# Kernel tuning notes

Hardware: AMD Instinct MI355X
Metric: run time of the kernel (lower is better)

Reference implementation:

```python
import jax, jax.numpy as jnp
import numpy as np

N_NODES = 10000
N_EDGES = 160000
N_GRAPHS = 64
IN_DIM, HID, HEADS, OUT_DIM = 128, 64, 8, 10
NEG_SLOPE = 0.2


def setup_inputs() -> dict:
    key = jax.random.key(0)
    ks = jax.random.split(key, 20)
    x = jax.random.normal(ks[0], (N_NODES, IN_DIM), dtype=jnp.float32)
    edge_index = jax.random.randint(ks[1], (2, N_EDGES), 0, N_NODES, dtype=jnp.int64)
    batch = jnp.sort(jax.random.randint(ks[2], (N_NODES,), 0, N_GRAPHS, dtype=jnp.int64))

    def glorot(k, shape):
        fan_in, fan_out = shape[0], shape[-1]
        lim = jnp.sqrt(6.0 / (fan_in + fan_out)).astype(jnp.float32)
        return jax.random.uniform(k, shape, jnp.float32, -lim, lim)

    d0 = HID * HEADS  # 512
    params = {
        # layer 0: IN_DIM -> HID x HEADS, concat
        'W0': glorot(ks[3], (IN_DIM, HEADS * HID)),
        'asrc0': glorot(ks[4], (HEADS, HID)), 'adst0': glorot(ks[5], (HEADS, HID)),
        'b0': jnp.zeros((HEADS * HID,), jnp.float32),
        # layer 1: 512 -> HID x HEADS, concat
        'W1': glorot(ks[6], (d0, HEADS * HID)),
        'asrc1': glorot(ks[7], (HEADS, HID)), 'adst1': glorot(ks[8], (HEADS, HID)),
        'b1': jnp.zeros((HEADS * HID,), jnp.float32),
        # layer 2: 512 -> HID, heads=1
        'W2': glorot(ks[9], (d0, HID)),
        'asrc2': glorot(ks[10], (1, HID)), 'adst2': glorot(ks[11], (1, HID)),
        'b2': jnp.zeros((HID,), jnp.float32),
        # classifier: 2*HID -> HID -> OUT_DIM
        'cW1': glorot(ks[12], (2 * HID, HID)), 'cb1': jnp.zeros((HID,), jnp.float32),
        'cW2': glorot(ks[13], (HID, OUT_DIM)), 'cb2': jnp.zeros((OUT_DIM,), jnp.float32),
    }
    return {'x': x, 'edge_index': edge_index, 'batch': batch, **params}


def gat_conv(h_in, src, dst, W, a_src, a_dst, b, heads, ch):
    # PyG GATConv (concat=True, negative_slope=0.2), dropout inactive (eval).
    N = h_in.shape[0]
    h = (h_in @ W).reshape(N, heads, ch)                       # [N,H,C]
    a_s = jnp.sum(h * a_src[None], axis=-1)                    # [N,H]
    a_d = jnp.sum(h * a_dst[None], axis=-1)                    # [N,H]
    e = jax.nn.leaky_relu(a_s[src] + a_d[dst], NEG_SLOPE)      # [E,H]
    # per-destination segment softmax (stable)
    m = jax.ops.segment_max(e, dst, num_segments=N)            # [N,H]
    ex = jnp.exp(e - m[dst])
    s = jax.ops.segment_sum(ex, dst, num_segments=N)
    alpha = ex / (s[dst] + 1e-16)                              # [E,H]
    out = jax.ops.segment_sum(h[src] * alpha[:, :, None], dst, num_segments=N)
    return out.reshape(N, heads * ch) + b


def _forward(x, src, dst, batch,
             W0, asrc0, adst0, b0, W1, asrc1, adst1, b1,
             W2, asrc2, adst2, b2, cW1, cb1, cW2, cb2):
    h = gat_conv(x, src, dst, W0, asrc0, adst0, b0, HEADS, HID)
    h = jax.nn.relu(h)
    h = gat_conv(h, src, dst, W1, asrc1, adst1, b1, HEADS, HID)
    h = jax.nn.relu(h)
    h = gat_conv(h, src, dst, W2, asrc2, adst2, b2, 1, HID)    # [N,HID]
    # global mean + max pool over graphs
    sums = jax.ops.segment_sum(h, batch, num_segments=N_GRAPHS)
    cnt = jax.ops.segment_sum(jnp.ones((h.shape[0], 1), h.dtype), batch, num_segments=N_GRAPHS)
    mean = sums / jnp.maximum(cnt, 1.0)
    mx = jax.ops.segment_max(h, batch, num_segments=N_GRAPHS)
    g = jnp.concatenate([mean, mx], axis=1)                    # [G, 2*HID]
    g = jax.nn.relu(g @ cW1 + cb1)
    return g @ cW2 + cb2                                       # [G, OUT_DIM]


def reference(x, edge_index, batch,
              W0, asrc0, adst0, b0, W1, asrc1, adst1, b1,
              W2, asrc2, adst2, b2, cW1, cb1, cW2, cb2):
    # PyG GATConv adds self-loops by default
    loops = jnp.arange(x.shape[0], dtype=edge_index.dtype)
    src = jnp.concatenate([edge_index[0], loops])
    dst = jnp.concatenate([edge_index[1], loops])
    return _forward(x, src, dst, batch,
                    W0, asrc0, adst0, b0, W1, asrc1, adst1, b1,
                    W2, asrc2, adst2, b2, cW1, cb1, cW2, cb2)
```

## Files before the change

### kernel.cpp

```cpp
#include <hip/hip_runtime.h>
#include <hip/hip_bf16.h>
#include <math.h>

#define NN 10000
#define EIN 160000
#define ETOT 170000
#define NG 64
#define INDIM 128
#define HID 64
#define HEADS 8
#define D0 512
#define OUTD 10

using bfrag = __attribute__((ext_vector_type(8))) short;
using ffrag = __attribute__((ext_vector_type(4))) float;

__device__ inline float bf2f(unsigned short u) { return __uint_as_float(((unsigned)u) << 16); }
__device__ inline unsigned short f2bf(float f) {
    __hip_bfloat16 b = __float2bfloat16(f);
    return *reinterpret_cast<unsigned short*>(&b);
}

__device__ void transpose_tile(const float* __restrict__ src, __hip_bfloat16* __restrict__ dst,
                               int R, int C, int bx, int by) {
    __shared__ float tile[32][33];
    int cb = bx * 32, rb = by * 32;
    int tx = threadIdx.x & 31, ty = threadIdx.x >> 5;
#pragma unroll
    for (int i = 0; i < 32; i += 8) {
        int r = rb + ty + i, c = cb + tx;
        tile[ty + i][tx] = (r < R && c < C) ? src[(size_t)r * C + c] : 0.f;
    }
    __syncthreads();
#pragma unroll
    for (int i = 0; i < 32; i += 8) {
        int c = cb + ty + i, r = rb + tx;
        if (c < C && r < R) dst[(size_t)c * R + r] = __float2bfloat16(tile[tx][ty + i]);
    }
}

__global__ __launch_bounds__(256) void prep_kernel(const float* __restrict__ x,
                                                   const float* __restrict__ W0,
                                                   const float* __restrict__ W1,
                                                   const float* __restrict__ W2,
                                                   __hip_bfloat16* __restrict__ xb,
                                                   __hip_bfloat16* __restrict__ W0T,
                                                   __hip_bfloat16* __restrict__ W1T,
                                                   __hip_bfloat16* __restrict__ W2T) {
    int bid = blockIdx.x;
    if (bid < 5000) {
        int i = bid * 256 + threadIdx.x;
        xb[i] = __float2bfloat16(x[i]);
    } else if (bid < 5064) {
        int lb = bid - 5000;
        transpose_tile(W0, W0T, INDIM, D0, lb & 15, lb >> 4);
    } else if (bid < 5320) {
        int lb = bid - 5064;
        transpose_tile(W1, W1T, D0, D0, lb & 15, lb >> 4);
    } else {
        int lb = bid - 5320;
        transpose_tile(W2, W2T, D0, 64, lb & 1, lb >> 1);
    }
}

__global__ void count_kernel(const int* __restrict__ ei, int* __restrict__ cnt) {
    int i = blockIdx.x * 256 + threadIdx.x;
    if (i >= ETOT) return;
    int dst = (i < EIN) ? ei[EIN + i] : (i - EIN);
    atomicAdd(&cnt[dst], 1);
}

__global__ __launch_bounds__(1024) void scan_kernel(const int* __restrict__ cnt,
                                                    int* __restrict__ row_ptr,
                                                    int* __restrict__ cursor) {
    __shared__ int ssum[1024];
    int t = threadIdx.x;
    const int PER = 10;
    int base = t * PER;
    int loc[PER];
    int s = 0;
#pragma unroll
    for (int i = 0; i < PER; i++) {
        int v = (base + i < NN) ? cnt[base + i] : 0;
        loc[i] = s; s += v;
    }
    ssum[t] = s;
    __syncthreads();
    for (int off = 1; off < 1024; off <<= 1) {
        int v = (t >= off) ? ssum[t - off] : 0;
        __syncthreads();
        ssum[t] += v;
        __syncthreads();
    }
    int bs = (t > 0) ? ssum[t - 1] : 0;
#pragma unroll
    for (int i = 0; i < PER; i++) {
        if (base + i < NN) { int v = bs + loc[i]; row_ptr[base + i] = v; cursor[base + i] = v; }
    }
    if (t == 0) row_ptr[NN] = ssum[1023];
}

__global__ void scatter_kernel(const int* __restrict__ ei, int* __restrict__ cursor,
                               int* __restrict__ col_src) {
    int i = blockIdx.x * 256 + threadIdx.x;
    if (i >= ETOT) return;
    int src, dst;
    if (i < EIN) { src = ei[i]; dst = ei[EIN + i]; }
    else { src = i - EIN; dst = src; }
    int pos = atomicAdd(&cursor[dst], 1);
    col_src[pos] = src;
}

#define GBM 128
#define GBN 128
#define GBK 32
#define LPAD 8

__global__ __launch_bounds__(256) void gemm_attn(const __hip_bfloat16* __restrict__ A,
                                                 const __hip_bfloat16* __restrict__ BT,
                                                 float* __restrict__ C,
                                                 __hip_bfloat16* __restrict__ Cb,
                                                 const float* __restrict__ asrc,
                                                 const float* __restrict__ adst,
                                                 float* __restrict__ a_s,
                                                 float* __restrict__ a_d,
                                                 int H, int M, int N, int K) {
    __shared__ __align__(16) short As[GBM][GBK + LPAD];
    __shared__ __align__(16) short Bs[GBN][GBK + LPAD];
    int tid = threadIdx.x;
    int wid = tid >> 6, lane = tid & 63;
    int wr = wid >> 1, wc = wid & 1;
    int brow = blockIdx.y * GBM, bcol = blockIdx.x * GBN;

    ffrag acc[4][4] = {};

    int srow = tid >> 2;
    int skq  = (tid & 3) * 8;

    int kq = (lane >> 4) * 8;
    int ra = lane & 15;

    for (int k0 = 0; k0 < K; k0 += GBK) {
#pragma unroll
        for (int p = 0; p < 2; ++p) {
            int r = srow + p * 64;
            int gr = brow + r;
            bfrag va = {0,0,0,0,0,0,0,0};
            if (gr < M) va = *(const bfrag*)(A + (size_t)gr * K + k0 + skq);
            *(bfrag*)&As[r][skq] = va;
            int gc = bcol + r;
            bfrag vb = {0,0,0,0,0,0,0,0};
            if (gc < N) vb = *(const bfrag*)(BT + (size_t)gc * K + k0 + skq);
            *(bfrag*)&Bs[r][skq] = vb;
        }
        __syncthreads();
        bfrag af[4], bf[4];
#pragma unroll
        for (int m = 0; m < 4; ++m) af[m] = *(const bfrag*)&As[wr * 64 + m * 16 + ra][kq];
#pragma unroll
        for (int n = 0; n < 4; ++n) bf[n] = *(const bfrag*)&Bs[wc * 64 + n * 16 + ra][kq];
#pragma unroll
        for (int m = 0; m < 4; ++m)
#pragma unroll
            for (int n = 0; n < 4; ++n)
                acc[m][n] = __builtin_amdgcn_mfma_f32_16x16x32_bf16(af[m], bf[n], acc[m][n], 0, 0, 0);
        __syncthreads();
    }

    int cr = (lane >> 4) * 4;
    int cc = lane & 15;

#pragma unroll
    for (int m = 0; m < 4; ++m) {
#pragma unroll
        for (int n = 0; n < 4; ++n) {
#pragma unroll
            for (int r = 0; r < 4; ++r) {
                int grow = brow + wr * 64 + m * 16 + cr + r;
                int gcol = bcol + wc * 64 + n * 16 + cc;
                if (grow < M && gcol < N) {
                    float v = acc[m][n][r];
                    if (C)  C[(size_t)grow * N + gcol] = v;
                    if (Cb) Cb[(size_t)grow * N + gcol] = __float2bfloat16(v);
                }
            }
        }
    }

    int head = (bcol >> 6) + wc;
    if (head < H) {
        float asl[4], adl[4];
        int cbase = head * 64;
#pragma unroll
        for (int n = 0; n < 4; ++n) {
            asl[n] = asrc[cbase + n * 16 + cc];
            adl[n] = adst[cbase + n * 16 + cc];
        }
#pragma unroll
        for (int m = 0; m < 4; ++m) {
#pragma unroll
            for (int r = 0; r < 4; ++r) {
                float ps = 0.f, pd = 0.f;
#pragma unroll
                for (int n = 0; n < 4; ++n) {
                    float av = acc[m][n][r];
                    ps += av * asl[n];
                    pd += av * adl[n];
                }
#pragma unroll
                for (int o = 1; o < 16; o <<= 1) {
                    ps += __shfl_xor(ps, o);
                    pd += __shfl_xor(pd, o);
                }
                if (cc == 0) {
                    int row = brow + wr * 64 + m * 16 + cr + r;
                    if (row < M) {
                        a_s[(size_t)row * H + head] = ps;
                        a_d[(size_t)row * H + head] = pd;
                    }
                }
            }
        }
    }
}

__global__ __launch_bounds__(256) void gat_agg8(const __hip_bfloat16* __restrict__ h,
                                                const float* __restrict__ a_s,
                                                const float* __restrict__ a_d,
                                                const int* __restrict__ row_ptr,
                                                const int* __restrict__ col_src,
                                                const float* __restrict__ bias,
                                                __hip_bfloat16* __restrict__ out)
{
    int n = blockIdx.x;
    int tid = threadIdx.x;
    int hh = tid >> 5;
    int c0 = tid * 2;
    int r0 = row_ptr[n], r1 = row_ptr[n + 1];
    float ad = a_d[n * 8 + hh];

    float acc0 = 0.f, acc1 = 0.f, ssum = 0.f;
    const unsigned short* hu = (const unsigned short*)h;
    for (int k = r0; k < r1; k += 8) {
        int kk[8]; int s[8]; float av[8]; unsigned v[8];
#pragma unroll
        for (int i = 0; i < 8; ++i) kk[i] = (k + i < r1) ? k + i : r1 - 1;
#pragma unroll
        for (int i = 0; i < 8; ++i) s[i] = col_src[kk[i]];
#pragma unroll
        for (int i = 0; i < 8; ++i) av[i] = a_s[s[i] * 8 + hh];
#pragma unroll
        for (int i = 0; i < 8; ++i) v[i] = *(const unsigned*)(hu + (size_t)s[i] * 512 + c0);
#pragma unroll
        for (int i = 0; i < 8; ++i) {
            float e = av[i] + ad;
            e = e > 0.f ? e : 0.2f * e;
            float al = __expf(e);
            al = (k + i < r1) ? al : 0.f;
            acc0 += al * bf2f((unsigned short)(v[i] & 0xffff));
            acc1 += al * bf2f((unsigned short)(v[i] >> 16));
            ssum += al;
        }
    }
    float inv = 1.f / (ssum + 1e-16f);
    float2 bv = *(const float2*)(bias + c0);
    float o0 = fmaxf(acc0 * inv + bv.x, 0.f);
    float o1 = fmaxf(acc1 * inv + bv.y, 0.f);
    unsigned pk = (unsigned)f2bf(o0) | ((unsigned)f2bf(o1) << 16);
    *(unsigned*)((unsigned short*)out + (size_t)n * 512 + c0) = pk;
}

__global__ __launch_bounds__(256) void gat_agg1(const float* __restrict__ h,
                                                const float* __restrict__ a_s,
                                                const float* __restrict__ a_d,
                                                const int* __restrict__ row_ptr,
                                                const int* __restrict__ col_src,
                                                const float* __restrict__ bias,
                                                float* __restrict__ out) {
    int n = blockIdx.x * 4 + (threadIdx.x >> 6);
    int lane = threadIdx.x & 63;
    if (n >= NN) return;
    int r0 = row_ptr[n], r1 = row_ptr[n + 1];
    float ad = a_d[n];
    float acc = 0.f, ssum = 0.f;
    for (int k = r0; k < r1; k += 8) {
        int kk[8]; int s[8]; float av[8]; float v[8];
#pragma unroll
        for (int i = 0; i < 8; ++i) kk[i] = (k + i < r1) ? k + i : r1 - 1;
#pragma unroll
        for (int i = 0; i < 8; ++i) s[i] = col_src[kk[i]];
#pragma unroll
        for (int i = 0; i < 8; ++i) av[i] = a_s[s[i]];
#pragma unroll
        for (int i = 0; i < 8; ++i) v[i] = h[(size_t)s[i] * 64 + lane];
#pragma unroll
        for (int i = 0; i < 8; ++i) {
            float e = av[i] + ad;
            e = e > 0.f ? e : 0.2f * e;
            float al = __expf(e);
            al = (k + i < r1) ? al : 0.f;
            acc += al * v[i];
            ssum += al;
        }
    }
    out[(size_t)n * 64 + lane] = acc / (ssum + 1e-16f) + bias[lane];
}

__global__ __launch_bounds__(256) void pool_classify(const float* __restrict__ h,
                                                     const int* __restrict__ batch,
                                                     const float* __restrict__ cW1, const float* __restrict__ cb1,
                                                     const float* __restrict__ cW2, const float* __restrict__ cb2,
                                                     float* __restrict__ out) {
    int g = blockIdx.x;
    int tid = threadIdx.x;
    int lane = tid & 63, w = tid >> 6;

    int lo = 0, hi = NN;
    while (lo < hi) { int mid = (lo + hi) >> 1; if (batch[mid] < g) lo = mid + 1; else hi = mid; }
    int s = lo;
    lo = s; hi = NN;
    while (lo < hi) { int mid = (lo + hi) >> 1; if (batch[mid] < g + 1) lo = mid + 1; else hi = mid; }
    int e = lo;

    float sum = 0.f, mx = -1e30f;
    for (int n = s + w; n < e; n += 4) {
        float v = h[(size_t)n * 64 + lane];
        sum += v; mx = fmaxf(mx, v);
    }
    __shared__ float ssum[4][64], smax[4][64];
    __shared__ float gv[128], c1[64];
    ssum[w][lane] = sum; smax[w][lane] = mx;
    __syncthreads();
    if (tid < 64) {
        float s4 = ssum[0][tid] + ssum[1][tid] + ssum[2][tid] + ssum[3][tid];
        float m4 = fmaxf(fmaxf(smax[0][tid], smax[1][tid]), fmaxf(smax[2][tid], smax[3][tid]));
        int cntv = e - s;
        float c = (float)(cntv > 1 ? cntv : 1);
        gv[tid] = s4 / c;
        gv[64 + tid] = m4;
    }
    __syncthreads();
    if (tid < 64) {
        float acc = cb1[tid];
        for (int k = 0; k < 128; k++) acc += gv[k] * cW1[k * 64 + tid];
        c1[tid] = fmaxf(acc, 0.f);
    }
    __syncthreads();
    if (tid < OUTD) {
        float o = cb2[tid];
        for (int k = 0; k < 64; k++) o += c1[k] * cW2[k * OUTD + tid];
        out[g * OUTD + tid] = o;
    }
}

extern "C" void kernel_launch(void* const* d_in, const int* in_sizes, int n_in,
                              void* d_out, int out_size, void* d_ws, size_t ws_size,
                              hipStream_t stream) {
    const float* x     = (const float*)d_in[0];
    const int*   ei    = (const int*)d_in[1];
    const int*   batch = (const int*)d_in[2];
    const float* W0    = (const float*)d_in[3];
    const float* asrc0 = (const float*)d_in[4];
    const float* adst0 = (const float*)d_in[5];
    const float* b0    = (const float*)d_in[6];
    const float* W1    = (const float*)d_in[7];
    const float* asrc1 = (const float*)d_in[8];
    const float* adst1 = (const float*)d_in[9];
    const float* b1    = (const float*)d_in[10];
    const float* W2    = (const float*)d_in[11];
    const float* asrc2 = (const float*)d_in[12];
    const float* adst2 = (const float*)d_in[13];
    const float* b2    = (const float*)d_in[14];
    const float* cW1   = (const float*)d_in[15];
    const float* cb1   = (const float*)d_in[16];
    const float* cW2   = (const float*)d_in[17];
    const float* cb2   = (const float*)d_in[18];
    float* out = (float*)d_out;

    char* ws = (char*)d_ws;
    size_t off = 0;
    auto alloc = [&](size_t bytes) { void* p = ws + off; off += (bytes + 255) & ~(size_t)255; return p; };
    __hip_bfloat16* bufAb = (__hip_bfloat16*)alloc((size_t)NN * D0 * 2);
    __hip_bfloat16* bufBb = (__hip_bfloat16*)alloc((size_t)NN * D0 * 2);
    float* bufC  = (float*)alloc((size_t)NN * 64 * 4);
    float* bufD  = (float*)alloc((size_t)NN * 64 * 4);
    __hip_bfloat16* xb   = (__hip_bfloat16*)alloc((size_t)NN * INDIM * 2);
    __hip_bfloat16* W0T  = (__hip_bfloat16*)alloc((size_t)D0 * INDIM * 2);
    __hip_bfloat16* W1T  = (__hip_bfloat16*)alloc((size_t)D0 * D0 * 2);
    __hip_bfloat16* W2T  = (__hip_bfloat16*)alloc((size_t)64 * D0 * 2);
    float* a_s     = (float*)alloc((size_t)NN * HEADS * 4);
    float* a_d     = (float*)alloc((size_t)NN * HEADS * 4);
    int*   cnt     = (int*)alloc((size_t)NN * 4);
    int*   row_ptr = (int*)alloc((size_t)(NN + 1) * 4);
    int*   cursor  = (int*)alloc((size_t)NN * 4);
    int*   col_src = (int*)alloc((size_t)(ETOT + 8) * 4);
    (void)ws_size; (void)n_in; (void)in_sizes; (void)out_size;

    prep_kernel<<<5352, 256, 0, stream>>>(x, W0, W1, W2, xb, W0T, W1T, W2T);

    hipMemsetAsync(cnt, 0, (size_t)NN * 4, stream);
    count_kernel<<<(ETOT + 255) / 256, 256, 0, stream>>>(ei, cnt);
    scan_kernel<<<1, 1024, 0, stream>>>(cnt, row_ptr, cursor);
    scatter_kernel<<<(ETOT + 255) / 256, 256, 0, stream>>>(ei, cursor, col_src);

    dim3 gg8(D0 / GBN, (NN + GBM - 1) / GBM);
    dim3 gg1(1, (NN + GBM - 1) / GBM);

    gemm_attn<<<gg8, 256, 0, stream>>>(xb, W0T, nullptr, bufAb, asrc0, adst0, a_s, a_d, HEADS, NN, D0, INDIM);
    gat_agg8<<<NN, 256, 0, stream>>>(bufAb, a_s, a_d, row_ptr, col_src, b0, bufBb);

    gemm_attn<<<gg8, 256, 0, stream>>>(bufBb, W1T, nullptr, bufAb, asrc1, adst1, a_s, a_d, HEADS, NN, D0, D0);
    gat_agg8<<<NN, 256, 0, stream>>>(bufAb, a_s, a_d, row_ptr, col_src, b1, bufBb);

    gemm_attn<<<gg1, 256, 0, stream>>>(bufBb, W2T, bufC, nullptr, asrc2, adst2, a_s, a_d, 1, NN, 64, D0);
    gat_agg1<<<(NN + 3) / 4, 256, 0, stream>>>(bufC, a_s, a_d, row_ptr, col_src, b2, bufD);

    pool_classify<<<NG, 256, 0, stream>>>(bufD, batch, cW1, cb1, cW2, cb2, out);
}
```

Before: 194.1 us.

## Shrink GEMM row tiles, split edge loops across two thread groups, use bf16 layer-2 features

The GEMM becomes a template on row fragments and is launched with 64-row tiles, giving more blocks on a problem with only 10000 rows. Both aggregation kernels double their thread count and split each node's edge list between two halves, then combine the partial sums in shared memory. This raises memory-level parallelism for low-degree nodes at the cost of an extra barrier and reduction. The layer-2 GEMM output is stored as bf16 to halve gather traffic, and the count buffer memset is folded into the prep kernel to drop one launch.

```diff
diff --git a/kernel.cpp b/kernel.cpp
--- a/kernel.cpp
+++ b/kernel.cpp
@@ -12,6 +12,9 @@
 #define D0 512
 #define OUTD 10
 
+#define GBK 32
+#define LPAD 8
+
 using bfrag = __attribute__((ext_vector_type(8))) short;
 using ffrag = __attribute__((ext_vector_type(4))) float;
 
@@ -46,7 +49,8 @@
                                                    __hip_bfloat16* __restrict__ xb,
                                                    __hip_bfloat16* __restrict__ W0T,
                                                    __hip_bfloat16* __restrict__ W1T,
-                                                   __hip_bfloat16* __restrict__ W2T) {
+                                                   __hip_bfloat16* __restrict__ W2T,
+                                                   int* __restrict__ cnt) {
     int bid = blockIdx.x;
     if (bid < 5000) {
         int i = bid * 256 + threadIdx.x;
@@ -57,9 +61,12 @@
     } else if (bid < 5320) {
         int lb = bid - 5064;
         transpose_tile(W1, W1T, D0, D0, lb & 15, lb >> 4);
-    } else {
+    } else if (bid < 5352) {
         int lb = bid - 5320;
         transpose_tile(W2, W2T, D0, 64, lb & 1, lb >> 1);
+    } else {
+        int i = (bid - 5352) * 256 + threadIdx.x;
+        if (i < NN) cnt[i] = 0;
     }
 }
 
@@ -111,11 +118,7 @@
     col_src[pos] = src;
 }
 
-#define GBM 128
-#define GBN 128
-#define GBK 32
-#define LPAD 8
-
+template <int FM>
 __global__ __launch_bounds__(256) void gemm_attn(const __hip_bfloat16* __restrict__ A,
                                                  const __hip_bfloat16* __restrict__ BT,
                                                  float* __restrict__ C,
@@ -125,14 +128,15 @@
                                                  float* __restrict__ a_s,
                                                  float* __restrict__ a_d,
                                                  int H, int M, int N, int K) {
-    __shared__ __align__(16) short As[GBM][GBK + LPAD];
-    __shared__ __align__(16) short Bs[GBN][GBK + LPAD];
+    constexpr int TM = 32 * FM;
+    __shared__ __align__(16) short As[TM][GBK + LPAD];
+    __shared__ __align__(16) short Bs[128][GBK + LPAD];
     int tid = threadIdx.x;
     int wid = tid >> 6, lane = tid & 63;
     int wr = wid >> 1, wc = wid & 1;
-    int brow = blockIdx.y * GBM, bcol = blockIdx.x * GBN;
-
-    ffrag acc[4][4] = {};
+    int brow = blockIdx.y * TM, bcol = blockIdx.x * 128;
+
+    ffrag acc[FM][4] = {};
 
     int srow = tid >> 2;
     int skq  = (tid & 3) * 8;
@@ -142,25 +146,31 @@
 
     for (int k0 = 0; k0 < K; k0 += GBK) {
 #pragma unroll
+        for (int p = 0; p < TM / 64 || p == 0; ++p) {
+            int r = srow + p * 64;
+            if (r < TM) {
+                int gr = brow + r;
+                bfrag va = {0,0,0,0,0,0,0,0};
+                if (gr < M) va = *(const bfrag*)(A + (size_t)gr * K + k0 + skq);
+                *(bfrag*)&As[r][skq] = va;
+            }
+        }
+#pragma unroll
         for (int p = 0; p < 2; ++p) {
             int r = srow + p * 64;
-            int gr = brow + r;
-            bfrag va = {0,0,0,0,0,0,0,0};
-            if (gr < M) va = *(const bfrag*)(A + (size_t)gr * K + k0 + skq);
-            *(bfrag*)&As[r][skq] = va;
             int gc = bcol + r;
             bfrag vb = {0,0,0,0,0,0,0,0};
             if (gc < N) vb = *(const bfrag*)(BT + (size_t)gc * K + k0 + skq);
             *(bfrag*)&Bs[r][skq] = vb;
         }
         __syncthreads();
-        bfrag af[4], bf[4];
-#pragma unroll
-        for (int m = 0; m < 4; ++m) af[m] = *(const bfrag*)&As[wr * 64 + m * 16 + ra][kq];
+        bfrag af[FM], bf[4];
+#pragma unroll
+        for (int m = 0; m < FM; ++m) af[m] = *(const bfrag*)&As[wr * (16 * FM) + m * 16 + ra][kq];
 #pragma unroll
         for (int n = 0; n < 4; ++n) bf[n] = *(const bfrag*)&Bs[wc * 64 + n * 16 + ra][kq];
 #pragma unroll
-        for (int m = 0; m < 4; ++m)
+        for (int m = 0; m < FM; ++m)
 #pragma unroll
             for (int n = 0; n < 4; ++n)
                 acc[m][n] = __builtin_amdgcn_mfma_f32_16x16x32_bf16(af[m], bf[n], acc[m][n], 0, 0, 0);
@@ -171,12 +181,12 @@
     int cc = lane & 15;
 
 #pragma unroll
-    for (int m = 0; m < 4; ++m) {
+    for (int m = 0; m < FM; ++m) {
 #pragma unroll
         for (int n = 0; n < 4; ++n) {
 #pragma unroll
             for (int r = 0; r < 4; ++r) {
-                int grow = brow + wr * 64 + m * 16 + cr + r;
+                int grow = brow + wr * (16 * FM) + m * 16 + cr + r;
                 int gcol = bcol + wc * 64 + n * 16 + cc;
                 if (grow < M && gcol < N) {
                     float v = acc[m][n][r];
@@ -197,7 +207,7 @@
             adl[n] = adst[cbase + n * 16 + cc];
         }
 #pragma unroll
-        for (int m = 0; m < 4; ++m) {
+        for (int m = 0; m < FM; ++m) {
 #pragma unroll
             for (int r = 0; r < 4; ++r) {
                 float ps = 0.f, pd = 0.f;
@@ -213,7 +223,7 @@
                     pd += __shfl_xor(pd, o);
                 }
                 if (cc == 0) {
-                    int row = brow + wr * 64 + m * 16 + cr + r;
+                    int row = brow + wr * (16 * FM) + m * 16 + cr + r;
                     if (row < M) {
                         a_s[(size_t)row * H + head] = ps;
                         a_d[(size_t)row * H + head] = pd;
@@ -224,7 +234,7 @@
     }
 }
 
-__global__ __launch_bounds__(256) void gat_agg8(const __hip_bfloat16* __restrict__ h,
+__global__ __launch_bounds__(512) void gat_agg8(const __hip_bfloat16* __restrict__ h,
                                                 const float* __restrict__ a_s,
                                                 const float* __restrict__ a_d,
                                                 const int* __restrict__ row_ptr,
@@ -234,17 +244,19 @@
 {
     int n = blockIdx.x;
     int tid = threadIdx.x;
-    int hh = tid >> 5;
-    int c0 = tid * 2;
+    int p = tid >> 8;
+    int t = tid & 255;
+    int hh = t >> 5;
+    int c0 = t * 2;
     int r0 = row_ptr[n], r1 = row_ptr[n + 1];
     float ad = a_d[n * 8 + hh];
 
-    float acc0 = 0.f, acc1 = 0.f, ssum = 0.f;
+    float acc0 = 0.f, acc1 = 0.f, ss = 0.f;
     const unsigned short* hu = (const unsigned short*)h;
-    for (int k = r0; k < r1; k += 8) {
+    for (int k = r0 + p; k < r1; k += 16) {
         int kk[8]; int s[8]; float av[8]; unsigned v[8];
 #pragma unroll
-        for (int i = 0; i < 8; ++i) kk[i] = (k + i < r1) ? k + i : r1 - 1;
+        for (int i = 0; i < 8; ++i) kk[i] = (k + 2 * i < r1) ? k + 2 * i : r1 - 1;
 #pragma unroll
         for (int i = 0; i < 8; ++i) s[i] = col_src[kk[i]];
 #pragma unroll
@@ -256,54 +268,76 @@
             float e = av[i] + ad;
             e = e > 0.f ? e : 0.2f * e;
             float al = __expf(e);
-            al = (k + i < r1) ? al : 0.f;
+            al = (k + 2 * i < r1) ? al : 0.f;
             acc0 += al * bf2f((unsigned short)(v[i] & 0xffff));
             acc1 += al * bf2f((unsigned short)(v[i] >> 16));
-            ssum += al;
-        }
-    }
-    float inv = 1.f / (ssum + 1e-16f);
-    float2 bv = *(const float2*)(bias + c0);
-    float o0 = fmaxf(acc0 * inv + bv.x, 0.f);
-    float o1 = fmaxf(acc1 * inv + bv.y, 0.f);
-    unsigned pk = (unsigned)f2bf(o0) | ((unsigned)f2bf(o1) << 16);
-    *(unsigned*)((unsigned short*)out + (size_t)n * 512 + c0) = pk;
-}
-
-__global__ __launch_bounds__(256) void gat_agg1(const float* __restrict__ h,
+            ss += al;
+        }
+    }
+    __shared__ float sa0[2][256], sa1[2][256], sss[2][256];
+    sa0[p][t] = acc0; sa1[p][t] = acc1; sss[p][t] = ss;
+    __syncthreads();
+    if (p == 0) {
+        float A0 = acc0 + sa0[1][t];
+        float A1 = acc1 + sa1[1][t];
+        float S  = ss + sss[1][t];
+        float inv = 1.f / (S + 1e-16f);
+        float2 bv = *(const float2*)(bias + c0);
+        float o0 = fmaxf(A0 * inv + bv.x, 0.f);
+        float o1 = fmaxf(A1 * inv + bv.y, 0.f);
+        unsigned pk = (unsigned)f2bf(o0) | ((unsigned)f2bf(o1) << 16);
+        *(unsigned*)((unsigned short*)out + (size_t)n * 512 + c0) = pk;
+    }
+}
+
+__global__ __launch_bounds__(512) void gat_agg1(const __hip_bfloat16* __restrict__ h,
                                                 const float* __restrict__ a_s,
                                                 const float* __restrict__ a_d,
                                                 const int* __restrict__ row_ptr,
                                                 const int* __restrict__ col_src,
                                                 const float* __restrict__ bias,
                                                 float* __restrict__ out) {
-    int n = blockIdx.x * 4 + (threadIdx.x >> 6);
-    int lane = threadIdx.x & 63;
-    if (n >= NN) return;
-    int r0 = row_ptr[n], r1 = row_ptr[n + 1];
-    float ad = a_d[n];
-    float acc = 0.f, ssum = 0.f;
-    for (int k = r0; k < r1; k += 8) {
-        int kk[8]; int s[8]; float av[8]; float v[8];
-#pragma unroll
-        for (int i = 0; i < 8; ++i) kk[i] = (k + i < r1) ? k + i : r1 - 1;
-#pragma unroll
-        for (int i = 0; i < 8; ++i) s[i] = col_src[kk[i]];
-#pragma unroll
-        for (int i = 0; i < 8; ++i) av[i] = a_s[s[i]];
-#pragma unroll
-        for (int i = 0; i < 8; ++i) v[i] = h[(size_t)s[i] * 64 + lane];
-#pragma unroll
-        for (int i = 0; i < 8; ++i) {
-            float e = av[i] + ad;
-            e = e > 0.f ? e : 0.2f * e;
-            float al = __expf(e);
-            al = (k + i < r1) ? al : 0.f;
-            acc += al * v[i];
-            ssum += al;
-        }
-    }
-    out[(size_t)n * 64 + lane] = acc / (ssum + 1e-16f) + bias[lane];
+    int tid = threadIdx.x;
+    int nod = tid >> 7;
+    int sub = tid & 127;
+    int p = sub >> 6, lane = sub & 63;
+    int n = blockIdx.x * 4 + nod;
+    __shared__ float sacc[4][2][64], sss[4][2][64];
+    float acc = 0.f, ss = 0.f;
+    int r0 = 0, r1 = 0;
+    float ad = 0.f;
+    if (n < NN) {
+        r0 = row_ptr[n]; r1 = row_ptr[n + 1];
+        ad = a_d[n];
+        const unsigned short* hu = (const unsigned short*)h;
+        for (int k = r0 + p; k < r1; k += 16) {
+            int kk[8]; int s[8]; float av[8]; float v[8];
+#pragma unroll
+            for (int i = 0; i < 8; ++i) kk[i] = (k + 2 * i < r1) ? k + 2 * i : r1 - 1;
+#pragma unroll
+            for (int i = 0; i < 8; ++i) s[i] = col_src[kk[i]];
+#pragma unroll
+            for (int i = 0; i < 8; ++i) av[i] = a_s[s[i]];
+#pragma unroll
+            for (int i = 0; i < 8; ++i) v[i] = bf2f(hu[(size_t)s[i] * 64 + lane]);
+#pragma unroll
+            for (int i = 0; i < 8; ++i) {
+                float e = av[i] + ad;
+                e = e > 0.f ? e : 0.2f * e;
+                float al = __expf(e);
+                al = (k + 2 * i < r1) ? al : 0.f;
+                acc += al * v[i];
+                ss += al;
+            }
+        }
+    }
+    sacc[nod][p][lane] = acc; sss[nod][p][lane] = ss;
+    __syncthreads();
+    if (p == 0 && n < NN) {
+        float A = acc + sacc[nod][1][lane];
+        float S = ss + sss[nod][1][lane];
+        out[(size_t)n * 64 + lane] = A / (S + 1e-16f) + bias[lane];
+    }
 }
 
 __global__ __launch_bounds__(256) void pool_classify(const float* __restrict__ h,
@@ -382,7 +416,7 @@
     auto alloc = [&](size_t bytes) { void* p = ws + off; off += (bytes + 255) & ~(size_t)255; return p; };
     __hip_bfloat16* bufAb = (__hip_bfloat16*)alloc((size_t)NN * D0 * 2);
     __hip_bfloat16* bufBb = (__hip_bfloat16*)alloc((size_t)NN * D0 * 2);
-    float* bufC  = (float*)alloc((size_t)NN * 64 * 4);
+    __hip_bfloat16* bufCb = (__hip_bfloat16*)alloc((size_t)NN * 64 * 2);
     float* bufD  = (float*)alloc((size_t)NN * 64 * 4);
     __hip_bfloat16* xb   = (__hip_bfloat16*)alloc((size_t)NN * INDIM * 2);
     __hip_bfloat16* W0T  = (__hip_bfloat16*)alloc((size_t)D0 * INDIM * 2);
@@ -396,24 +430,23 @@
     int*   col_src = (int*)alloc((size_t)(ETOT + 8) * 4);
     (void)ws_size; (void)n_in; (void)in_sizes; (void)out_size;
 
-    prep_kernel<<<5352, 256, 0, stream>>>(x, W0, W1, W2, xb, W0T, W1T, W2T);
-
-    hipMemsetAsync(cnt, 0, (size_t)NN * 4, stream);
+    prep_kernel<<<5392, 256, 0, stream>>>(x, W0, W1, W2, xb, W0T, W1T, W2T, cnt);
+
     count_kernel<<<(ETOT + 255) / 256, 256, 0, stream>>>(ei, cnt);
     scan_kernel<<<1, 1024, 0, stream>>>(cnt, row_ptr, cursor);
     scatter_kernel<<<(ETOT + 255) / 256, 256, 0, stream>>>(ei, cursor, col_src);
 
-    dim3 gg8(D0 / GBN, (NN + GBM - 1) / GBM);
-    dim3 gg1(1, (NN + GBM - 1) / GBM);
-
-    gemm_attn<<<gg8, 256, 0, stream>>>(xb, W0T, nullptr, bufAb, asrc0, adst0, a_s, a_d, HEADS, NN, D0, INDIM);
-    gat_agg8<<<NN, 256, 0, stream>>>(bufAb, a_s, a_d, row_ptr, col_src, b0, bufBb);
-
-    gemm_attn<<<gg8, 256, 0, stream>>>(bufBb, W1T, nullptr, bufAb, asrc1, adst1, a_s, a_d, HEADS, NN, D0, D0);
-    gat_agg8<<<NN, 256, 0, stream>>>(bufAb, a_s, a_d, row_ptr, col_src, b1, bufBb);
-
-    gemm_attn<<<gg1, 256, 0, stream>>>(bufBb, W2T, bufC, nullptr, asrc2, adst2, a_s, a_d, 1, NN, 64, D0);
-    gat_agg1<<<(NN + 3) / 4, 256, 0, stream>>>(bufC, a_s, a_d, row_ptr, col_src, b2, bufD);
+    dim3 gg8(D0 / 128, (NN + 63) / 64);
+    dim3 gg1(1, (NN + 63) / 64);
+
+    gemm_attn<2><<<gg8, 256, 0, stream>>>(xb, W0T, nullptr, bufAb, asrc0, adst0, a_s, a_d, HEADS, NN, D0, INDIM);
+    gat_agg8<<<NN, 512, 0, stream>>>(bufAb, a_s, a_d, row_ptr, col_src, b0, bufBb);
+
+    gemm_attn<2><<<gg8, 256, 0, stream>>>(bufBb, W1T, nullptr, bufAb, asrc1, adst1, a_s, a_d, HEADS, NN, D0, D0);
+    gat_agg8<<<NN, 512, 0, stream>>>(bufAb, a_s, a_d, row_ptr, col_src, b1, bufBb);
+
+    gemm_attn<2><<<gg1, 256, 0, stream>>>(bufBb, W2T, nullptr, bufCb, asrc2, adst2, a_s, a_d, 1, NN, 64, D0);
+    gat_agg1<<<(NN + 3) / 4, 512, 0, stream>>>(bufCb, a_s, a_d, row_ptr, col_src, b2, bufD);
 
     pool_classify<<<NG, 256, 0, stream>>>(bufD, batch, cW1, cb1, cW2, cb2, out);
 }
```

Measured after the change: 211.3 us. 8.9% more time.
